# Optimization experiments

Hardware: AMD Instinct MI355X
Metric: run time of the kernel (lower is better)

## Reference

```python
import jax, jax.numpy as jnp
import numpy as np

B, S, C, H = 256, 512, 512, 512
MOG_ITERS = 5


def _xavier(key, shape):
    fan_out, fan_in = shape
    lim = float(np.sqrt(6.0 / (fan_in + fan_out)))
    return jax.random.uniform(key, shape, minval=-lim, maxval=lim, dtype=jnp.float32)


def setup_inputs() -> dict:
    key = jax.random.key(0)
    ks = jax.random.split(key, 7)
    x = jax.random.normal(ks[0], (B, S, C), dtype=jnp.float32)
    return {
        "x": x,
        "Wih_w": _xavier(ks[1], (4 * H, C)), "Wih_b": jnp.zeros((4 * H,), jnp.float32),
        "Wmx_w": _xavier(ks[2], (H, C)),     "Wmx_b": jnp.zeros((H,), jnp.float32),
        "Wmh_w": _xavier(ks[3], (H, H)),     "Wmh_b": jnp.zeros((H,), jnp.float32),
        "Whm_w": _xavier(ks[4], (4 * H, H)), "Whm_b": jnp.zeros((4 * H,), jnp.float32),
        "Q": _xavier(ks[5], (H, C)),
        "R": _xavier(ks[6], (C, H)),
    }


def _mogrify(xt, ht, Q, R):
    # alternating mogrifier rounds; odd i updates xt, even i updates ht
    for i in range(1, MOG_ITERS + 1):
        if i % 2 == 1:
            xt = 2.0 * jax.nn.sigmoid(ht @ Q) * xt  # (B,H)@(H,C) -> (B,C)
        else:
            ht = 2.0 * jax.nn.sigmoid(xt @ R) * ht  # (B,C)@(C,H) -> (B,H)
    return xt, ht


def reference(x, Wih_w, Wih_b, Wmx_w, Wmx_b, Wmh_w, Wmh_b, Whm_w, Whm_b, Q, R):
    batch = x.shape[0]
    h0 = jnp.zeros((batch, H), x.dtype)
    c0 = jnp.zeros((batch, H), x.dtype)

    def step(carry, xt):
        ht, Ct = carry
        xt, ht = _mogrify(xt, ht, Q, R)
        mt = xt @ Wmx_w.T + Wmx_b + ht @ Wmh_w.T + Wmh_b          # (B,H)
        gates = xt @ Wih_w.T + Wih_b + mt @ Whm_w.T + Whm_b        # (B,4H)
        i_g, f_g, g_g, o_g = jnp.split(gates, 4, axis=1)
        Ct = jax.nn.sigmoid(f_g) * Ct + jax.nn.sigmoid(i_g) * jnp.tanh(g_g)
        ht = jax.nn.sigmoid(o_g) * jnp.tanh(Ct)
        return (ht, Ct), ht

    xs = jnp.swapaxes(x, 0, 1)                  # (S,B,C)
    _, hs = jax.lax.scan(step, (h0, c0), xs)    # (S,B,H)
    return jnp.swapaxes(hs, 0, 1)               # (B,S,H)
```

## Files before the change

### kernel.cpp

```cpp
#include <hip/hip_runtime.h>

#define Bdim 256
#define Sdim 512
#define Cdim 512
#define Hdim 512
#define NP 16
#define NSLICE 16

typedef __attribute__((ext_vector_type(8))) short bfrag;
typedef __attribute__((ext_vector_type(8))) unsigned short u16x8;
typedef __attribute__((ext_vector_type(4))) float f32x4;

__device__ __forceinline__ unsigned short f2bf_rne(float f) {
    union { float f; unsigned u; } v; v.f = f;
    return (unsigned short)((v.u + 0x7fffu + ((v.u >> 16) & 1u)) >> 16);
}
__device__ __forceinline__ float sigmoidf_(float x) { return 1.0f / (1.0f + __expf(-x)); }

template<bool TRANS>
__global__ __launch_bounds__(256) void pack_weight(const float* __restrict__ src,
                                                   unsigned short* __restrict__ dst,
                                                   int K, int N) {
    int tid = blockIdx.x * 256 + threadIdx.x;
    int total = (K >> 5) * (N >> 4) * 64;
    if (tid >= total) return;
    int lane = tid & 63;
    int blk  = tid >> 6;
    int kc   = blk & 15;
    int n16  = blk >> 4;
    int n  = (n16 << 4) + (lane & 15);
    int kb = (kc << 5) + ((lane >> 4) << 3);
    u16x8 v;
#pragma unroll
    for (int j = 0; j < 8; ++j) {
        int k = kb + j;
        float f = TRANS ? src[(size_t)n * K + k] : src[(size_t)k * N + n];
        v[j] = f2bf_rne(f);
    }
    *(u16x8*)(dst + ((size_t)tid << 3)) = v;
}

__global__ __launch_bounds__(256) void weff_kernel(const float* __restrict__ A,
                                                   const float* __restrict__ Whm,
                                                   const float* __restrict__ Wadd,
                                                   float* __restrict__ C) {
    int n = blockIdx.x;
    int k = blockIdx.y * 256 + threadIdx.x;
    const float* wrow = Whm + (size_t)n * 512;
    float acc = 0.f;
#pragma unroll 8
    for (int j = 0; j < 512; ++j) acc += A[(size_t)j * 512 + k] * wrow[j];
    if (Wadd) acc += Wadd[(size_t)n * 512 + k];
    C[(size_t)k * 2048 + n] = acc;
}

__global__ __launch_bounds__(256) void beff_kernel(const float* __restrict__ bmx,
                                                   const float* __restrict__ bmh,
                                                   const float* __restrict__ Whm,
                                                   const float* __restrict__ bih,
                                                   const float* __restrict__ bhm,
                                                   float* __restrict__ beff) {
    int n = blockIdx.x * 256 + threadIdx.x;
    const float* wrow = Whm + (size_t)n * 512;
    float acc = bih[n] + bhm[n];
#pragma unroll 8
    for (int j = 0; j < 512; ++j) acc += (bmx[j] + bmh[j]) * wrow[j];
    beff[n] = acc;
}

__global__ __launch_bounds__(256) void init_state(unsigned short* __restrict__ Hg,
                                                  unsigned short* __restrict__ Hm,
                                                  int* __restrict__ flags) {
    int tid = blockIdx.x * 256 + threadIdx.x;
    if (tid < NP * NSLICE) flags[tid] = 0;
    for (int i = tid; i < NP * 8192; i += gridDim.x * 256) { Hg[i] = 0; Hm[i] = 0; }
}


__device__ __forceinline__ bfrag afrag_load(const unsigned short* F, int kc, int lane) {
    union { unsigned long long u[2]; bfrag f; } v;
    const unsigned long long* pp = (const unsigned long long*)(F + kc * 512 + lane * 8);
    v.u[0] = __hip_atomic_load(pp,     __ATOMIC_RELAXED, __HIP_MEMORY_SCOPE_AGENT);
    v.u[1] = __hip_atomic_load(pp + 1, __ATOMIC_RELAXED, __HIP_MEMORY_SCOPE_AGENT);
    return v.f;
}

__device__ __forceinline__ void store_pair(unsigned short* Dst, int m, int n,
                                           unsigned short b, int lane) {
    unsigned pb = __shfl_xor((unsigned)b, 1);
    if (!(lane & 1)) {
        unsigned word = (unsigned)b | (pb << 16);
        int idx = ((n >> 5) << 9) + (((m & 15) + ((n >> 3) & 3) * 16) << 3) + (n & 7);
        __hip_atomic_store((unsigned*)(Dst + idx), word,
                           __ATOMIC_RELAXED, __HIP_MEMORY_SCOPE_AGENT);
    }
}

__device__ __forceinline__ void wait_flags(const int* fl, int target, int lane) {
    while (true) {
        int f = __hip_atomic_load(fl + (lane & 15), __ATOMIC_RELAXED, __HIP_MEMORY_SCOPE_AGENT);
        if (__all(f >= target)) break;
        __builtin_amdgcn_s_sleep(1);
    }
    asm volatile("" ::: "memory");
}

__device__ __forceinline__ void post_flag(int* fl, int s, int qnew, int lane) {
    asm volatile("s_waitcnt vmcnt(0)" ::: "memory");
    if (lane == 0)
        __hip_atomic_store(fl + s, qnew, __ATOMIC_RELAXED, __HIP_MEMORY_SCOPE_AGENT);
}

__device__ __forceinline__ void mog_stage(const unsigned short* __restrict__ Af,
                                          const unsigned short* __restrict__ Wp,
                                          unsigned short* __restrict__ Dst,
                                          float pv[2][4],
                                          int s, int lane, int lm, int lq) {
    f32x4 acc[2] = {};
    const bfrag* B = (const bfrag*)Wp + (size_t)s * 2048 + lane;
#pragma unroll 8
    for (int kc = 0; kc < 16; ++kc) {
        bfrag a = afrag_load(Af, kc, lane);
        acc[0] = __builtin_amdgcn_mfma_f32_16x16x32_bf16(a, B[kc * 64],        acc[0], 0, 0, 0);
        acc[1] = __builtin_amdgcn_mfma_f32_16x16x32_bf16(a, B[1024 + kc * 64], acc[1], 0, 0, 0);
    }
#pragma unroll
    for (int nt = 0; nt < 2; ++nt)
#pragma unroll
        for (int r = 0; r < 4; ++r) {
            int n = s * 32 + nt * 16 + lm;
            int m = lq * 4 + r;
            float v = 2.0f * sigmoidf_(acc[nt][r]) * pv[nt][r];
            pv[nt][r] = v;
            store_pair(Dst, m, n, f2bf_rne(v), lane);
        }
}

__global__ __launch_bounds__(64)
void moglstm_persistent(const float* __restrict__ x,
                        const unsigned short* __restrict__ Qp,
                        const unsigned short* __restrict__ Rp,
                        const unsigned short* __restrict__ WXp,
                        const unsigned short* __restrict__ WHp,
                        const float* __restrict__ beff,
                        unsigned short* __restrict__ Xb,
                        unsigned short* __restrict__ Hmb,
                        unsigned short* __restrict__ Hgb,
                        int* __restrict__ flags,
                        float* __restrict__ out) {
    const int w = blockIdx.x;
    const int p = w >> 4, s = w & 15;
    const int lane = threadIdx.x & 63, lm = lane & 15, lq = lane >> 4;
    unsigned short* Xp = Xb + p * 8192;
    unsigned short* Hm = Hmb + p * 8192;
    unsigned short* Hg = Hgb + p * 8192;
    int* fl = flags + p * NSLICE;

    float px[2][4];
    float ph[2][4] = {};
    float cst[2][4] = {};
    float bia[4][2];
#pragma unroll
    for (int g = 0; g < 4; ++g)
#pragma unroll
        for (int nt = 0; nt < 2; ++nt)
            bia[g][nt] = beff[g * 512 + s * 32 + nt * 16 + lm];

    const size_t xbase = (size_t)(p * 16) * Sdim * Cdim;
    const size_t obase = (size_t)(p * 16) * Sdim * Hdim;

    int q = 0;
#pragma unroll 1
    for (int t = 0; t < Sdim; ++t) {
#pragma unroll
        for (int nt = 0; nt < 2; ++nt)
#pragma unroll
            for (int r = 0; r < 4; ++r) {
                int n = s * 32 + nt * 16 + lm;
                int m = lq * 4 + r;
                px[nt][r] = x[xbase + (size_t)m * (Sdim * Cdim) + (size_t)t * Cdim + n];
            }
        wait_flags(fl, q, lane);
        mog_stage(Hg, Qp, Xp, px, s, lane, lm, lq);
        post_flag(fl, s, ++q, lane);
        wait_flags(fl, q, lane);
        mog_stage(Xp, Rp, Hm, ph, s, lane, lm, lq);
        post_flag(fl, s, ++q, lane);
        wait_flags(fl, q, lane);
        mog_stage(Hm, Qp, Xp, px, s, lane, lm, lq);
        post_flag(fl, s, ++q, lane);
        wait_flags(fl, q, lane);
        mog_stage(Xp, Rp, Hm, ph, s, lane, lm, lq);
        post_flag(fl, s, ++q, lane);
        wait_flags(fl, q, lane);
        mog_stage(Hm, Qp, Xp, px, s, lane, lm, lq);
        post_flag(fl, s, ++q, lane);
        wait_flags(fl, q, lane);
        {
            f32x4 acc[4][2] = {};
#pragma unroll 4
            for (int kc = 0; kc < 16; ++kc) {
                bfrag aX = afrag_load(Xp, kc, lane);
                bfrag aH = afrag_load(Hm, kc, lane);
#pragma unroll
                for (int g = 0; g < 4; ++g) {
                    const bfrag* BX = (const bfrag*)WXp + (size_t)((g * 32 + s * 2) * 16 + kc) * 64 + lane;
                    const bfrag* BH = (const bfrag*)WHp + (size_t)((g * 32 + s * 2) * 16 + kc) * 64 + lane;
                    acc[g][0] = __builtin_amdgcn_mfma_f32_16x16x32_bf16(aX, BX[0],    acc[g][0], 0, 0, 0);
                    acc[g][0] = __builtin_amdgcn_mfma_f32_16x16x32_bf16(aH, BH[0],    acc[g][0], 0, 0, 0);
                    acc[g][1] = __builtin_amdgcn_mfma_f32_16x16x32_bf16(aX, BX[1024], acc[g][1], 0, 0, 0);
                    acc[g][1] = __builtin_amdgcn_mfma_f32_16x16x32_bf16(aH, BH[1024], acc[g][1], 0, 0, 0);
                }
            }
#pragma unroll
            for (int nt = 0; nt < 2; ++nt)
#pragma unroll
                for (int r = 0; r < 4; ++r) {
                    int n = s * 32 + nt * 16 + lm;
                    int m = lq * 4 + r;
                    float ig = sigmoidf_(acc[0][nt][r] + bia[0][nt]);
                    float fg = sigmoidf_(acc[1][nt][r] + bia[1][nt]);
                    float gg = tanhf(acc[2][nt][r] + bia[2][nt]);
                    float og = sigmoidf_(acc[3][nt][r] + bia[3][nt]);
                    float c = fg * cst[nt][r] + ig * gg;
                    cst[nt][r] = c;
                    float h = og * tanhf(c);
                    ph[nt][r] = h;
                    store_pair(Hg, m, n, f2bf_rne(h), lane);
                    out[obase + (size_t)m * (Sdim * Hdim) + (size_t)t * Hdim + n] = h;
                }
        }
        post_flag(fl, s, ++q, lane);
    }
}

extern "C" void kernel_launch(void* const* d_in, const int* in_sizes, int n_in,
                              void* d_out, int out_size, void* d_ws, size_t ws_size,
                              hipStream_t stream) {
    const float* x     = (const float*)d_in[0];
    const float* Wih_w = (const float*)d_in[1];
    const float* Wih_b = (const float*)d_in[2];
    const float* Wmx_w = (const float*)d_in[3];
    const float* Wmx_b = (const float*)d_in[4];
    const float* Wmh_w = (const float*)d_in[5];
    const float* Wmh_b = (const float*)d_in[6];
    const float* Whm_w = (const float*)d_in[7];
    const float* Whm_b = (const float*)d_in[8];
    const float* Q     = (const float*)d_in[9];
    const float* R     = (const float*)d_in[10];
    float* out = (float*)d_out;

    unsigned short* packQ  = (unsigned short*)d_ws;
    unsigned short* packR  = packQ  + 512 * 512;
    unsigned short* packWX = packR  + 512 * 512;
    unsigned short* packWH = packWX + 512 * 2048;
    unsigned short* Xb  = packWH + 512 * 2048;
    unsigned short* Hmb = Xb  + NP * 8192;
    unsigned short* Hgb = Hmb + NP * 8192;
    float* beff    = (float*)(Hgb + NP * 8192);
    float* scratch = beff + 2048;
    int* flags     = (int*)(scratch + 512 * 2048);

    pack_weight<false><<<dim3(128), dim3(256), 0, stream>>>(Q, packQ, 512, 512);
    pack_weight<false><<<dim3(128), dim3(256), 0, stream>>>(R, packR, 512, 512);
    weff_kernel<<<dim3(2048, 2), dim3(256), 0, stream>>>(Wmx_w, Whm_w, Wih_w, scratch);
    pack_weight<false><<<dim3(512), dim3(256), 0, stream>>>(scratch, packWX, 512, 2048);
    weff_kernel<<<dim3(2048, 2), dim3(256), 0, stream>>>(Wmh_w, Whm_w, nullptr, scratch);
    pack_weight<false><<<dim3(512), dim3(256), 0, stream>>>(scratch, packWH, 512, 2048);
    beff_kernel<<<dim3(8), dim3(256), 0, stream>>>(Wmx_b, Wmh_b, Whm_w, Wih_b, Whm_b, beff);
    init_state<<<dim3(128), dim3(256), 0, stream>>>(Hgb, Hmb, flags);

    moglstm_persistent<<<dim3(NP * NSLICE), dim3(64), 0, stream>>>(
        x, packQ, packR, packWX, packWH, beff, Xb, Hmb, Hgb, flags, out);
}
```

Measured before the change: 30.93 ms.

## Replace flag barriers with sequence-tagged data words polled directly by consumers

Drops the per-stage flag arrays, the flag wait loop and the vmcnt(0)-then-post handshake. Each pair of bf16 activations is now stored as a 64-bit word whose upper half carries a stage sequence number. Consumers spin on the data itself until every fragment shows the expected tag, so they can start as soon as their own inputs arrive instead of waiting for a full group barrier. The final gate GEMM is split into an X pass and an M pass with separate validation. The cost is twice the bytes for the activation buffers and heavier, data-dependent polling loops that need more registers.

```diff
diff --git a/kernel.cpp b/kernel.cpp
--- a/kernel.cpp
+++ b/kernel.cpp
@@ -10,6 +10,7 @@
 typedef __attribute__((ext_vector_type(8))) short bfrag;
 typedef __attribute__((ext_vector_type(8))) unsigned short u16x8;
 typedef __attribute__((ext_vector_type(4))) float f32x4;
+typedef unsigned long long u64;
 
 __device__ __forceinline__ unsigned short f2bf_rne(float f) {
     union { float f; unsigned u; } v; v.f = f;
@@ -68,61 +69,65 @@
     beff[n] = acc;
 }
 
-__global__ __launch_bounds__(256) void init_state(unsigned short* __restrict__ Hg,
-                                                  unsigned short* __restrict__ Hm,
-                                                  int* __restrict__ flags) {
+__global__ __launch_bounds__(256) void init_state(u64* __restrict__ Gc) {
     int tid = blockIdx.x * 256 + threadIdx.x;
-    if (tid < NP * NSLICE) flags[tid] = 0;
-    for (int i = tid; i < NP * 8192; i += gridDim.x * 256) { Hg[i] = 0; Hm[i] = 0; }
-}
-
-
-__device__ __forceinline__ bfrag afrag_load(const unsigned short* F, int kc, int lane) {
-    union { unsigned long long u[2]; bfrag f; } v;
-    const unsigned long long* pp = (const unsigned long long*)(F + kc * 512 + lane * 8);
-    v.u[0] = __hip_atomic_load(pp,     __ATOMIC_RELAXED, __HIP_MEMORY_SCOPE_AGENT);
-    v.u[1] = __hip_atomic_load(pp + 1, __ATOMIC_RELAXED, __HIP_MEMORY_SCOPE_AGENT);
-    return v.f;
-}
-
-__device__ __forceinline__ void store_pair(unsigned short* Dst, int m, int n,
-                                           unsigned short b, int lane) {
-    unsigned pb = __shfl_xor((unsigned)b, 1);
+    for (int i = tid; i < NP * 4096; i += gridDim.x * 256) Gc[i] = 0ull;
+}
+
+
+__device__ __forceinline__ void validate16(u64 (*aw)[4], const u64* __restrict__ base,
+                                           unsigned q) {
+    unsigned inv = 0xFFFFu;
+    while (inv) {
+#pragma unroll
+        for (int kc = 0; kc < 16; ++kc) {
+            if (inv & (1u << kc)) {
+#pragma unroll
+                for (int wd = 0; wd < 4; ++wd)
+                    aw[kc][wd] = __hip_atomic_load(base + kc * 16 + wd,
+                                                   __ATOMIC_RELAXED, __HIP_MEMORY_SCOPE_AGENT);
+            }
+        }
+        unsigned next = 0;
+#pragma unroll
+        for (int kc = 0; kc < 16; ++kc) {
+            if (inv & (1u << kc)) {
+                bool ok = (unsigned)(aw[kc][0] >> 32) == q && (unsigned)(aw[kc][1] >> 32) == q
+                       && (unsigned)(aw[kc][2] >> 32) == q && (unsigned)(aw[kc][3] >> 32) == q;
+                if (!ok) next |= 1u << kc;
+            }
+        }
+        inv = next;
+    }
+}
+
+__device__ __forceinline__ void store_tagged(u64* __restrict__ Dc, int m, int n,
+                                             unsigned short b, unsigned q, int lane) {
+    unsigned ub = b;
+    unsigned pb = __shfl_xor(ub, 1);
     if (!(lane & 1)) {
-        unsigned word = (unsigned)b | (pb << 16);
-        int idx = ((n >> 5) << 9) + (((m & 15) + ((n >> 3) & 3) * 16) << 3) + (n & 7);
-        __hip_atomic_store((unsigned*)(Dst + idx), word,
+        u64 word = (u64)(ub | (pb << 16)) | ((u64)q << 32);
+        __hip_atomic_store(Dc + m * 256 + (n >> 1), word,
                            __ATOMIC_RELAXED, __HIP_MEMORY_SCOPE_AGENT);
     }
 }
 
-__device__ __forceinline__ void wait_flags(const int* fl, int target, int lane) {
-    while (true) {
-        int f = __hip_atomic_load(fl + (lane & 15), __ATOMIC_RELAXED, __HIP_MEMORY_SCOPE_AGENT);
-        if (__all(f >= target)) break;
-        __builtin_amdgcn_s_sleep(1);
-    }
-    asm volatile("" ::: "memory");
-}
-
-__device__ __forceinline__ void post_flag(int* fl, int s, int qnew, int lane) {
-    asm volatile("s_waitcnt vmcnt(0)" ::: "memory");
-    if (lane == 0)
-        __hip_atomic_store(fl + s, qnew, __ATOMIC_RELAXED, __HIP_MEMORY_SCOPE_AGENT);
-}
-
-__device__ __forceinline__ void mog_stage(const unsigned short* __restrict__ Af,
-                                          const unsigned short* __restrict__ Wp,
-                                          unsigned short* __restrict__ Dst,
+__device__ __forceinline__ void mog_stage(const u64* __restrict__ Ac,
+                                          const bfrag* __restrict__ B,
+                                          u64* __restrict__ Dc,
                                           float pv[2][4],
+                                          unsigned q_in, unsigned q_out,
                                           int s, int lane, int lm, int lq) {
+    u64 aw[16][4];
+    validate16(aw, Ac + lm * 256 + lq * 4, q_in);
     f32x4 acc[2] = {};
-    const bfrag* B = (const bfrag*)Wp + (size_t)s * 2048 + lane;
-#pragma unroll 8
+#pragma unroll
     for (int kc = 0; kc < 16; ++kc) {
-        bfrag a = afrag_load(Af, kc, lane);
-        acc[0] = __builtin_amdgcn_mfma_f32_16x16x32_bf16(a, B[kc * 64],        acc[0], 0, 0, 0);
-        acc[1] = __builtin_amdgcn_mfma_f32_16x16x32_bf16(a, B[1024 + kc * 64], acc[1], 0, 0, 0);
+        union { unsigned u[4]; bfrag f; } A;
+#pragma unroll
+        for (int wd = 0; wd < 4; ++wd) A.u[wd] = (unsigned)aw[kc][wd];
+        acc[0] = __builtin_amdgcn_mfma_f32_16x16x32_bf16(A.f, B[kc * 64],        acc[0], 0, 0, 0);
+        acc[1] = __builtin_amdgcn_mfma_f32_16x16x32_bf16(A.f, B[1024 + kc * 64], acc[1], 0, 0, 0);
     }
 #pragma unroll
     for (int nt = 0; nt < 2; ++nt)
@@ -132,29 +137,30 @@
             int m = lq * 4 + r;
             float v = 2.0f * sigmoidf_(acc[nt][r]) * pv[nt][r];
             pv[nt][r] = v;
-            store_pair(Dst, m, n, f2bf_rne(v), lane);
-        }
-}
-
-__global__ __launch_bounds__(64)
+            store_tagged(Dc, m, n, f2bf_rne(v), q_out, lane);
+        }
+}
+
+__global__ __launch_bounds__(64, 1)
 void moglstm_persistent(const float* __restrict__ x,
                         const unsigned short* __restrict__ Qp,
                         const unsigned short* __restrict__ Rp,
                         const unsigned short* __restrict__ WXp,
                         const unsigned short* __restrict__ WHp,
                         const float* __restrict__ beff,
-                        unsigned short* __restrict__ Xb,
-                        unsigned short* __restrict__ Hmb,
-                        unsigned short* __restrict__ Hgb,
-                        int* __restrict__ flags,
+                        u64* __restrict__ Xcb,
+                        u64* __restrict__ Mcb,
+                        u64* __restrict__ Gcb,
                         float* __restrict__ out) {
     const int w = blockIdx.x;
     const int p = w >> 4, s = w & 15;
     const int lane = threadIdx.x & 63, lm = lane & 15, lq = lane >> 4;
-    unsigned short* Xp = Xb + p * 8192;
-    unsigned short* Hm = Hmb + p * 8192;
-    unsigned short* Hg = Hgb + p * 8192;
-    int* fl = flags + p * NSLICE;
+    u64* Xc = Xcb + p * 4096;
+    u64* Mc = Mcb + p * 4096;
+    u64* Gc = Gcb + p * 4096;
+
+    const bfrag* BQ = (const bfrag*)Qp + (size_t)s * 2048 + lane;
+    const bfrag* BR = (const bfrag*)Rp + (size_t)s * 2048 + lane;
 
     float px[2][4];
     float ph[2][4] = {};
@@ -169,9 +175,9 @@
     const size_t xbase = (size_t)(p * 16) * Sdim * Cdim;
     const size_t obase = (size_t)(p * 16) * Sdim * Hdim;
 
-    int q = 0;
 #pragma unroll 1
     for (int t = 0; t < Sdim; ++t) {
+        const unsigned q0 = 6u * (unsigned)t;
 #pragma unroll
         for (int nt = 0; nt < 2; ++nt)
 #pragma unroll
@@ -180,36 +186,38 @@
                 int m = lq * 4 + r;
                 px[nt][r] = x[xbase + (size_t)m * (Sdim * Cdim) + (size_t)t * Cdim + n];
             }
-        wait_flags(fl, q, lane);
-        mog_stage(Hg, Qp, Xp, px, s, lane, lm, lq);
-        post_flag(fl, s, ++q, lane);
-        wait_flags(fl, q, lane);
-        mog_stage(Xp, Rp, Hm, ph, s, lane, lm, lq);
-        post_flag(fl, s, ++q, lane);
-        wait_flags(fl, q, lane);
-        mog_stage(Hm, Qp, Xp, px, s, lane, lm, lq);
-        post_flag(fl, s, ++q, lane);
-        wait_flags(fl, q, lane);
-        mog_stage(Xp, Rp, Hm, ph, s, lane, lm, lq);
-        post_flag(fl, s, ++q, lane);
-        wait_flags(fl, q, lane);
-        mog_stage(Hm, Qp, Xp, px, s, lane, lm, lq);
-        post_flag(fl, s, ++q, lane);
-        wait_flags(fl, q, lane);
+        mog_stage(Gc, BQ, Xc, px, q0,     q0 + 1, s, lane, lm, lq);
+        mog_stage(Xc, BR, Mc, ph, q0 + 1, q0 + 2, s, lane, lm, lq);
+        mog_stage(Mc, BQ, Xc, px, q0 + 2, q0 + 3, s, lane, lm, lq);
+        mog_stage(Xc, BR, Mc, ph, q0 + 3, q0 + 4, s, lane, lm, lq);
+        mog_stage(Mc, BQ, Xc, px, q0 + 4, q0 + 5, s, lane, lm, lq);
         {
             f32x4 acc[4][2] = {};
-#pragma unroll 4
+            u64 aw[16][4];
+            validate16(aw, Xc + lm * 256 + lq * 4, q0 + 5);
+#pragma unroll
             for (int kc = 0; kc < 16; ++kc) {
-                bfrag aX = afrag_load(Xp, kc, lane);
-                bfrag aH = afrag_load(Hm, kc, lane);
+                union { unsigned u[4]; bfrag f; } A;
+#pragma unroll
+                for (int wd = 0; wd < 4; ++wd) A.u[wd] = (unsigned)aw[kc][wd];
 #pragma unroll
                 for (int g = 0; g < 4; ++g) {
-                    const bfrag* BX = (const bfrag*)WXp + (size_t)((g * 32 + s * 2) * 16 + kc) * 64 + lane;
-                    const bfrag* BH = (const bfrag*)WHp + (size_t)((g * 32 + s * 2) * 16 + kc) * 64 + lane;
-                    acc[g][0] = __builtin_amdgcn_mfma_f32_16x16x32_bf16(aX, BX[0],    acc[g][0], 0, 0, 0);
-                    acc[g][0] = __builtin_amdgcn_mfma_f32_16x16x32_bf16(aH, BH[0],    acc[g][0], 0, 0, 0);
-                    acc[g][1] = __builtin_amdgcn_mfma_f32_16x16x32_bf16(aX, BX[1024], acc[g][1], 0, 0, 0);
-                    acc[g][1] = __builtin_amdgcn_mfma_f32_16x16x32_bf16(aH, BH[1024], acc[g][1], 0, 0, 0);
+                    const bfrag* BX = (const bfrag*)WXp + ((size_t)((g * 32 + s * 2) * 16 + kc)) * 64 + lane;
+                    acc[g][0] = __builtin_amdgcn_mfma_f32_16x16x32_bf16(A.f, BX[0],    acc[g][0], 0, 0, 0);
+                    acc[g][1] = __builtin_amdgcn_mfma_f32_16x16x32_bf16(A.f, BX[1024], acc[g][1], 0, 0, 0);
+                }
+            }
+            validate16(aw, Mc + lm * 256 + lq * 4, q0 + 4);
+#pragma unroll
+            for (int kc = 0; kc < 16; ++kc) {
+                union { unsigned u[4]; bfrag f; } A;
+#pragma unroll
+                for (int wd = 0; wd < 4; ++wd) A.u[wd] = (unsigned)aw[kc][wd];
+#pragma unroll
+                for (int g = 0; g < 4; ++g) {
+                    const bfrag* BH = (const bfrag*)WHp + ((size_t)((g * 32 + s * 2) * 16 + kc)) * 64 + lane;
+                    acc[g][0] = __builtin_amdgcn_mfma_f32_16x16x32_bf16(A.f, BH[0],    acc[g][0], 0, 0, 0);
+                    acc[g][1] = __builtin_amdgcn_mfma_f32_16x16x32_bf16(A.f, BH[1024], acc[g][1], 0, 0, 0);
                 }
             }
 #pragma unroll
@@ -226,11 +234,10 @@
                     cst[nt][r] = c;
                     float h = og * tanhf(c);
                     ph[nt][r] = h;
-                    store_pair(Hg, m, n, f2bf_rne(h), lane);
+                    store_tagged(Gc, m, n, f2bf_rne(h), q0 + 6, lane);
                     out[obase + (size_t)m * (Sdim * Hdim) + (size_t)t * Hdim + n] = h;
                 }
         }
-        post_flag(fl, s, ++q, lane);
     }
 }
 
@@ -254,12 +261,11 @@
     unsigned short* packR  = packQ  + 512 * 512;
     unsigned short* packWX = packR  + 512 * 512;
     unsigned short* packWH = packWX + 512 * 2048;
-    unsigned short* Xb  = packWH + 512 * 2048;
-    unsigned short* Hmb = Xb  + NP * 8192;
-    unsigned short* Hgb = Hmb + NP * 8192;
-    float* beff    = (float*)(Hgb + NP * 8192);
+    u64* Xcb = (u64*)(packWH + 512 * 2048);
+    u64* Mcb = Xcb + NP * 4096;
+    u64* Gcb = Mcb + NP * 4096;
+    float* beff    = (float*)(Gcb + NP * 4096);
     float* scratch = beff + 2048;
-    int* flags     = (int*)(scratch + 512 * 2048);
 
     pack_weight<false><<<dim3(128), dim3(256), 0, stream>>>(Q, packQ, 512, 512);
     pack_weight<false><<<dim3(128), dim3(256), 0, stream>>>(R, packR, 512, 512);
@@ -268,8 +274,8 @@
     weff_kernel<<<dim3(2048, 2), dim3(256), 0, stream>>>(Wmh_w, Whm_w, nullptr, scratch);
     pack_weight<false><<<dim3(512), dim3(256), 0, stream>>>(scratch, packWH, 512, 2048);
     beff_kernel<<<dim3(8), dim3(256), 0, stream>>>(Wmx_b, Wmh_b, Whm_w, Wih_b, Whm_b, beff);
-    init_state<<<dim3(128), dim3(256), 0, stream>>>(Hgb, Hmb, flags);
+    init_state<<<dim3(64), dim3(256), 0, stream>>>(Gcb);
 
     moglstm_persistent<<<dim3(NP * NSLICE), dim3(64), 0, stream>>>(
-        x, packQ, packR, packWX, packWH, beff, Xb, Hmb, Hgb, flags, out);
-}
+        x, packQ, packR, packWX, packWH, beff, Xcb, Mcb, Gcb, out);
+}
```

Result: slower. 64.70 ms (+109.2%).
